# Performance work log

Hardware: AMD Instinct MI355X
Metric: run time of the kernel (lower is better)

## Reference

```python
import jax, jax.numpy as jnp
import numpy as np

B, S, D, H, F = 2, 2048, 1024, 16, 4096
DK = D // H
EPS = 1e-6


def _ln(x, g, b):
    mu = jnp.mean(x, axis=-1, keepdims=True)
    var = jnp.mean(jnp.square(x - mu), axis=-1, keepdims=True)
    return (x - mu) * jax.lax.rsqrt(var + EPS) * g + b


def setup_inputs() -> dict:
    key = jax.random.key(0)
    ks = jax.random.split(key, 8)
    sc = 0.02
    return {
        "x": jax.random.normal(ks[0], (B, S, D), jnp.float32),
        "wq": jax.random.normal(ks[1], (D, D), jnp.float32) * sc,
        "bq": jnp.zeros((D,), jnp.float32),
        "wk": jax.random.normal(ks[2], (D, D), jnp.float32) * sc,
        "bk": jnp.zeros((D,), jnp.float32),
        "wv": jax.random.normal(ks[3], (D, D), jnp.float32) * sc,
        "bv": jnp.zeros((D,), jnp.float32),
        "wo": jax.random.normal(ks[4], (D, D), jnp.float32) * sc,
        "bo": jnp.zeros((D,), jnp.float32),
        "w1": jax.random.normal(ks[5], (D, F), jnp.float32) * sc,
        "b1": jnp.zeros((F,), jnp.float32),
        "w2": jax.random.normal(ks[6], (F, D), jnp.float32) * sc,
        "b2": jnp.zeros((D,), jnp.float32),
        "g1": jnp.ones((D,), jnp.float32),
        "be1": jnp.zeros((D,), jnp.float32),
        "g2": jnp.ones((D,), jnp.float32),
        "be2": jnp.zeros((D,), jnp.float32),
    }


def reference(x, wq, bq, wk, bk, wv, bv, wo, bo, w1, b1, w2, b2, g1, be1, g2, be2):
    # Multi-head self-attention (no masks, eval-mode dropout = identity)
    q = (x @ wq + bq).reshape(B, S, H, DK)
    k = (x @ wk + bk).reshape(B, S, H, DK)
    v = (x @ wv + bv).reshape(B, S, H, DK)
    scale = 1.0 / (DK ** 0.5)
    score = jnp.einsum('bihd,bjhd->bhij', q, k) * scale  # [B,H,S,S]
    p = jax.nn.softmax(score, axis=-1)
    attn = jnp.einsum('bhij,bjhd->bihd', p, v).reshape(B, S, D)
    attn = attn @ wo + bo
    # residual + LayerNorm 1
    h = _ln(x + attn, g1, be1)
    # FFN (relu) + residual + LayerNorm 2
    ff = jax.nn.relu(h @ w1 + b1) @ w2 + b2
    return _ln(h + ff, g2, be2)
```

## Files before the change

kernel.cpp:

```cpp
#include <hip/hip_runtime.h>
#include <hip/hip_bf16.h>
#include <cmath>

typedef __bf16 bf16_t;
typedef __bf16 bf16x4 __attribute__((ext_vector_type(4)));
typedef __bf16 bf16x8 __attribute__((ext_vector_type(8)));
typedef float  f32x4  __attribute__((ext_vector_type(4)));

__device__ __forceinline__ void gld_lds16(const bf16_t* g, bf16_t* l) {
    __builtin_amdgcn_global_load_lds(
        (const __attribute__((address_space(1))) void*)g,
        (__attribute__((address_space(3))) void*)l,
        16, 0, 0);
}

struct PrepArgs {
    const float* w[6]; bf16_t* wt[6];
    int K[6], N[6], start[6];
    const float* x; bf16_t* xb; int castStart;
    const float* bq; const float* bk; float* bqkv; int biasStart;
};

__global__ __launch_bounds__(256) void prep(PrepArgs pa) {
    __shared__ float tile[32][33];
    const int bid = blockIdx.x, t = threadIdx.x;
    if (bid < pa.castStart) {
        int mi = 0;
#pragma unroll
        for (int i = 1; i < 6; i++) if (bid >= pa.start[i]) mi = i;
        const int tt  = bid - pa.start[mi];
        const int nbx = pa.N[mi] >> 5;
        const int n0 = (tt % nbx) * 32, k0 = (tt / nbx) * 32;
        const float* in = pa.w[mi];
        bf16_t* out = pa.wt[mi];
        const int K = pa.K[mi], N = pa.N[mi];
        const int tx = t & 31, ty = t >> 5;
#pragma unroll
        for (int i = 0; i < 4; i++) {
            int kk = ty + i * 8;
            tile[kk][tx] = in[(size_t)(k0 + kk) * N + n0 + tx];
        }
        __syncthreads();
#pragma unroll
        for (int i = 0; i < 4; i++) {
            int nn = ty + i * 8;
            out[(size_t)(n0 + nn) * K + k0 + tx] = (bf16_t)tile[tx][nn];
        }
    } else if (bid < pa.biasStart) {
        int i = (bid - pa.castStart) * 256 + t;
        f32x4 v = ((const f32x4*)pa.x)[i];
        bf16x4 o;
        o[0] = (bf16_t)v[0]; o[1] = (bf16_t)v[1]; o[2] = (bf16_t)v[2]; o[3] = (bf16_t)v[3];
        ((bf16x4*)pa.xb)[i] = o;
    } else {
#pragma unroll
        for (int j = 0; j < 8; j++) {
            int idx = t * 8 + j;
            pa.bqkv[idx] = idx < 1024 ? pa.bq[idx] : pa.bk[idx - 1024];
        }
    }
}

struct GemmDesc {
    const bf16_t* A; const bf16_t* Bt; const float* bias;
    float* Cf; bf16_t* Cb;
    int M, N, lda, Kloc, relu, nbn, bias_row;
    long bt_bstride, c_bstride;
    int scale_cols; float scale;
};

template<int MT>
__device__ __forceinline__ void gemm_core(const GemmDesc& d, int bidx, int batch,
                                          int kh, bf16_t* As, bf16_t* Bs) {
    constexpr int TM = MT * 32;
    const int tid  = threadIdx.x;
    const int lane = tid & 63;
    const int wave = tid >> 6;
    const int wm = wave & 1, wn = wave >> 1;

    const int span  = 8 * d.nbn;
    const int group = bidx / span;
    const int rem   = bidx % span;
    const int bm    = group * 8 + (rem & 7);
    const int bn    = rem >> 3;

    const bf16_t* Bt_b = d.Bt + (size_t)batch * d.bt_bstride;
    float*  Cf_b = d.Cf ? d.Cf + (size_t)batch * d.c_bstride + (size_t)kh * d.M * d.N : nullptr;
    bf16_t* Cb_b = d.Cb ? d.Cb + (size_t)batch * d.c_bstride : nullptr;
    const int koff = kh * d.Kloc;

    const int r4 = tid >> 2;
    const int kc = (tid & 3) * 8;
    const bf16_t* Ag = d.A  + (size_t)(bm * TM  + r4) * d.lda + koff + kc;
    const bf16_t* Bg = Bt_b + (size_t)(bn * 128 + r4) * d.lda + koff + kc;

    f32x4 acc[MT][4] = {};
    const int mrow = lane & 15;
    const int q8   = (lane >> 4) * 8;

    for (int k0 = 0; k0 < d.Kloc; k0 += 64) {
        __syncthreads();
#pragma unroll
        for (int hh = 0; hh < 2; hh++) {
#pragma unroll
            for (int i = 0; i < MT / 2; i++)
                gld_lds16(Ag + (size_t)(i * 64) * d.lda + k0 + hh * 32,
                          As + hh * (TM * 32) + i * 64 * 32 + tid * 8);
            gld_lds16(Bg + k0 + hh * 32,                      Bs + hh * 4096 + tid * 8);
            gld_lds16(Bg + (size_t)64 * d.lda + k0 + hh * 32, Bs + hh * 4096 + 64 * 32 + tid * 8);
        }
        __syncthreads();

#pragma unroll
        for (int hh = 0; hh < 2; hh++) {
            bf16x8 af[MT], bfr[4];
#pragma unroll
            for (int mt = 0; mt < MT; mt++)
                af[mt] = *(const bf16x8*)(As + hh * (TM * 32) +
                                          (wm * (MT * 16) + mt * 16 + mrow) * 32 + q8);
#pragma unroll
            for (int nt = 0; nt < 4; nt++)
                bfr[nt] = *(const bf16x8*)(Bs + hh * 4096 +
                                           (wn * 64 + nt * 16 + mrow) * 32 + q8);
#pragma unroll
            for (int mt = 0; mt < MT; mt++)
#pragma unroll
                for (int nt = 0; nt < 4; nt++)
                    acc[mt][nt] = __builtin_amdgcn_mfma_f32_16x16x32_bf16(
                        af[mt], bfr[nt], acc[mt][nt], 0, 0, 0);
        }
    }

    const int rq = (lane >> 4) * 4;
#pragma unroll
    for (int mt = 0; mt < MT; mt++) {
        int row0 = bm * TM + wm * (MT * 16) + mt * 16 + rq;
#pragma unroll
        for (int nt = 0; nt < 4; nt++) {
            int col = bn * 128 + wn * 64 + nt * 16 + mrow;
            float bvc = (d.bias && kh == 0 && !d.bias_row) ? d.bias[col] : 0.f;
            float sc = (col < d.scale_cols) ? d.scale : 1.f;
#pragma unroll
            for (int r = 0; r < 4; r++) {
                float bb = (d.bias && kh == 0 && d.bias_row) ? d.bias[row0 + r] : bvc;
                float v = acc[mt][nt][r] + bb;
                if (d.relu) v = fmaxf(v, 0.f);
                v *= sc;
                size_t idx = (size_t)(row0 + r) * d.N + col;
                if (Cf_b) Cf_b[idx] = v;
                if (Cb_b) Cb_b[idx] = (bf16_t)v;
            }
        }
    }
}

template<int MT>
__global__ __launch_bounds__(256) void gemm_bt(GemmDesc d) {
    __shared__ __attribute__((aligned(16))) bf16_t As[2 * MT * 32 * 32];
    __shared__ __attribute__((aligned(16))) bf16_t Bs[2 * 128 * 32];
    gemm_core<MT>(d, blockIdx.x, blockIdx.y, blockIdx.z, As, Bs);
}

__global__ __launch_bounds__(256) void gemm_dual(GemmDesc d0, int nblocks0,
                                                 GemmDesc d1, int nblocks1) {
    __shared__ __attribute__((aligned(16))) bf16_t As[2 * 128 * 32];
    __shared__ __attribute__((aligned(16))) bf16_t Bs[2 * 128 * 32];
    const int bid = blockIdx.x;
    if (bid < nblocks0) {
        gemm_core<4>(d0, bid, 0, 0, As, Bs);
    } else {
        int b2 = bid - nblocks0;
        gemm_core<4>(d1, b2 % nblocks1, b2 / nblocks1, 0, As, Bs);
    }
}

__global__ __launch_bounds__(512) void flash_attn_mfma(
    const bf16_t* __restrict__ QKb,
    const bf16_t* __restrict__ Vtg,
    bf16_t* __restrict__ Outb) {
    __shared__ __attribute__((aligned(16))) bf16_t QPs[128 * 72];
    __shared__ __attribute__((aligned(16))) bf16_t Ks[2][64 * 32];
    __shared__ __attribute__((aligned(16))) bf16_t Vs[2][64 * 32];
    const int t = threadIdx.x;
    const int lane = t & 63, wave = t >> 6;
    const int g = lane >> 4, cl = lane & 15;
    const int b = blockIdx.z, h = blockIdx.y, q0 = blockIdx.x * 128;
    const int RS = 2048;
    const bf16_t* Qg = QKb + (size_t)(b * 2048 + q0) * RS + h * 64;
    const bf16_t* Kg = QKb + (size_t)(b * 2048) * RS + 1024 + h * 64;
    const bf16_t* Vg = Vtg + ((size_t)b * 1024 + h * 64) * 2048;

    {
        int qr = t >> 2, qc = (t & 3) * 8;
        gld_lds16(Qg + (size_t)qr * RS + qc,      QPs + t * 8);
        gld_lds16(Qg + (size_t)qr * RS + 32 + qc, QPs + 4096 + t * 8);
    }
    const int kr = (t & 255) >> 2;
    const int kc = (t & 3) * 8;
    const int khf = (t >> 8) * 32;

    f32x4 Oacc[4] = {};
    f32x4 Lacc = {};
    bf16x8 ones;
#pragma unroll
    for (int j = 0; j < 8; j++) ones[j] = (bf16_t)1.0f;

    const int qrow_s = (wave * 16 + cl) * 32 + g * 8;
    const int prow_w = (wave * 16 + cl) * 72;

    __syncthreads();
    const bf16x8 bq0 = *(const bf16x8*)(QPs + qrow_s);
    const bf16x8 bq1 = *(const bf16x8*)(QPs + 4096 + qrow_s);

    for (int kt = 0; kt < 2048; kt += 64) {
        __syncthreads();
        gld_lds16(Kg + (size_t)(kt + kr) * RS + khf + kc,  (bf16_t*)Ks + t * 8);
        gld_lds16(Vg + (size_t)kr * 2048 + kt + khf + kc,  (bf16_t*)Vs + t * 8);
        __syncthreads();

        f32x4 Sacc[4] = {};
#pragma unroll
        for (int ks = 0; ks < 2; ks++) {
            const bf16x8 bq = ks ? bq1 : bq0;
#pragma unroll
            for (int mt = 0; mt < 4; mt++) {
                bf16x8 ak = *(const bf16x8*)(&Ks[ks][(mt * 16 + cl) * 32 + g * 8]);
                Sacc[mt] = __builtin_amdgcn_mfma_f32_16x16x32_bf16(ak, bq, Sacc[mt], 0, 0, 0);
            }
        }

#pragma unroll
        for (int mt = 0; mt < 4; mt++) {
            bf16x4 p4;
#pragma unroll
            for (int r = 0; r < 4; r++)
                p4[r] = (bf16_t)__builtin_amdgcn_exp2f(Sacc[mt][r]);
            *(bf16x4*)(QPs + prow_w + mt * 16 + g * 4) = p4;
        }

#pragma unroll
        for (int ks = 0; ks < 2; ks++) {
            bf16x8 ap = *(const bf16x8*)(QPs + prow_w + ks * 32 + g * 8);
            Lacc = __builtin_amdgcn_mfma_f32_16x16x32_bf16(ap, ones, Lacc, 0, 0, 0);
#pragma unroll
            for (int nt = 0; nt < 4; nt++) {
                bf16x8 bv = *(const bf16x8*)(&Vs[ks][(nt * 16 + cl) * 32 + g * 8]);
                Oacc[nt] = __builtin_amdgcn_mfma_f32_16x16x32_bf16(ap, bv, Oacc[nt], 0, 0, 0);
            }
        }
    }

#pragma unroll
    for (int r = 0; r < 4; r++) {
        float inv = 1.f / Lacc[r];
        int qrow = q0 + wave * 16 + g * 4 + r;
        size_t base = (size_t)(b * 2048 + qrow) * 1024 + h * 64;
#pragma unroll
        for (int nt = 0; nt < 4; nt++)
            Outb[base + nt * 16 + cl] = (bf16_t)(Oacc[nt][r] * inv);
    }
}

__global__ __launch_bounds__(256) void resid_ln3(const float* __restrict__ a,
                                                 const float* __restrict__ p0,
                                                 const float* __restrict__ p1,
                                                 const float* __restrict__ g,
                                                 const float* __restrict__ be,
                                                 float* __restrict__ outf,
                                                 bf16_t* __restrict__ outb) {
    const int row = blockIdx.x, t = threadIdx.x;
    const size_t base = (size_t)row * 1024;
    f32x4 v = ((const f32x4*)(a + base))[t] + ((const f32x4*)(p0 + base))[t];
    if (p1) v += ((const f32x4*)(p1 + base))[t];
    float sum = v[0] + v[1] + v[2] + v[3];
    float sq  = v[0] * v[0] + v[1] * v[1] + v[2] * v[2] + v[3] * v[3];
#pragma unroll
    for (int o = 1; o < 64; o <<= 1) {
        sum += __shfl_xor(sum, o);
        sq  += __shfl_xor(sq, o);
    }
    __shared__ float red[8];
    int wave = t >> 6, lane = t & 63;
    if (lane == 0) { red[wave] = sum; red[4 + wave] = sq; }
    __syncthreads();
    sum = red[0] + red[1] + red[2] + red[3];
    sq  = red[4] + red[5] + red[6] + red[7];
    float mu  = sum * (1.f / 1024.f);
    float var = sq * (1.f / 1024.f) - mu * mu;
    float rs  = rsqrtf(var + 1e-6f);
    f32x4 g4 = ((const f32x4*)g)[t];
    f32x4 b4 = ((const f32x4*)be)[t];
    f32x4 o = (v - mu) * rs * g4 + b4;
    ((f32x4*)(outf + base))[t] = o;
    if (outb) {
        bf16x4 ob;
        ob[0] = (bf16_t)o[0]; ob[1] = (bf16_t)o[1]; ob[2] = (bf16_t)o[2]; ob[3] = (bf16_t)o[3];
        ((bf16x4*)(outb + base))[t] = ob;
    }
}

extern "C" void kernel_launch(void* const* d_in, const int* in_sizes, int n_in,
                              void* d_out, int out_size, void* d_ws, size_t ws_size,
                              hipStream_t stream) {
    (void)in_sizes; (void)n_in; (void)out_size; (void)ws_size;
    const float* x   = (const float*)d_in[0];
    const float* wq  = (const float*)d_in[1];
    const float* bq  = (const float*)d_in[2];
    const float* wk  = (const float*)d_in[3];
    const float* bk  = (const float*)d_in[4];
    const float* wv  = (const float*)d_in[5];
    const float* bv  = (const float*)d_in[6];
    const float* wo  = (const float*)d_in[7];
    const float* bo  = (const float*)d_in[8];
    const float* w1  = (const float*)d_in[9];
    const float* b1  = (const float*)d_in[10];
    const float* w2  = (const float*)d_in[11];
    const float* b2  = (const float*)d_in[12];
    const float* g1  = (const float*)d_in[13];
    const float* be1 = (const float*)d_in[14];
    const float* g2  = (const float*)d_in[15];
    const float* be2 = (const float*)d_in[16];
    float* out = (float*)d_out;

    char* ws = (char*)d_ws;
    const size_t MB = 1ull << 20;
    bf16_t* xb    = (bf16_t*)(ws + 0);
    bf16_t* WtQKV = (bf16_t*)(ws + 8 * MB);
    bf16_t* WtO   = (bf16_t*)(ws + 14 * MB);
    bf16_t* Wt1   = (bf16_t*)(ws + 16 * MB);
    bf16_t* Wt2   = (bf16_t*)(ws + 24 * MB);
    float*  bqkv  = (float*)(ws + 32 * MB);
    bf16_t* QKb   = (bf16_t*)(ws + 33 * MB);
    bf16_t* Vt    = (bf16_t*)(ws + 49 * MB);
    bf16_t* ffb   = (bf16_t*)(ws + 33 * MB);
    float*  oa    = (float*)(ws + 65 * MB);
    float*  f2    = (float*)(ws + 65 * MB);
    float*  hbuf  = (float*)(ws + 97 * MB);
    bf16_t* hb    = (bf16_t*)(ws + 113 * MB);
    bf16_t* ab    = xb;
    const int MN = 4096 * 1024;
    const float Cs = 0.125f * 1.4426950408889634f;

    PrepArgs pa;
    pa.w[0] = wq; pa.w[1] = wk; pa.w[2] = wv; pa.w[3] = wo; pa.w[4] = w1; pa.w[5] = w2;
    pa.wt[0] = WtQKV; pa.wt[1] = WtQKV + 1024 * 1024; pa.wt[2] = WtQKV + 2048 * 1024;
    pa.wt[3] = WtO; pa.wt[4] = Wt1; pa.wt[5] = Wt2;
    int Ksz[6] = {1024, 1024, 1024, 1024, 1024, 4096};
    int Nsz[6] = {1024, 1024, 1024, 1024, 4096, 1024};
    int st[6]  = {0, 1024, 2048, 3072, 4096, 8192};
    for (int i = 0; i < 6; i++) { pa.K[i] = Ksz[i]; pa.N[i] = Nsz[i]; pa.start[i] = st[i]; }
    pa.x = x; pa.xb = xb; pa.castStart = 12288;
    pa.bq = bq; pa.bk = bk; pa.bqkv = bqkv; pa.biasStart = 12288 + 4096;
    prep<<<12288 + 4096 + 1, 256, 0, stream>>>(pa);

    GemmDesc dqk = { xb, WtQKV, bqkv, nullptr, QKb,
                     4096, 2048, 1024, 1024, 0, 16, 0, 0, 0, 1024, Cs };
    GemmDesc dv  = { WtQKV + 2048 * 1024, xb, bv, nullptr, Vt,
                     1024, 2048, 1024, 1024, 0, 16, 1,
                     (long)2048 * 1024, (long)1024 * 2048, 0, 1.f };
    gemm_dual<<<768, 256, 0, stream>>>(dqk, 512, dv, 128);

    flash_attn_mfma<<<dim3(16, 16, 2), 512, 0, stream>>>(QKb, Vt, ab);

    GemmDesc dwo = { ab, WtO, bo, oa, nullptr,
                     4096, 1024, 1024, 512, 0, 8, 0, 0, 0, 0, 1.f };
    gemm_bt<4><<<dim3(256, 1, 2), 256, 0, stream>>>(dwo);

    resid_ln3<<<4096, 256, 0, stream>>>(x, oa, oa + MN, g1, be1, hbuf, hb);

    GemmDesc df1 = { hb, Wt1, b1, nullptr, ffb,
                     4096, 4096, 1024, 1024, 1, 32, 0, 0, 0, 0, 1.f };
    gemm_bt<4><<<1024, 256, 0, stream>>>(df1);

    GemmDesc df2 = { ffb, Wt2, b2, f2, nullptr,
                     4096, 1024, 4096, 2048, 0, 8, 0, 0, 0, 0, 1.f };
    gemm_bt<4><<<dim3(256, 1, 2), 256, 0, stream>>>(df2);

    resid_ln3<<<4096, 256, 0, stream>>>(hbuf, f2, f2 + MN, g2, be2, out, nullptr);
}
```

Before: 418.7 us.

## Prefetch next GEMM K-tile into registers while computing current tile

Replaces the direct global-to-LDS loads with register prefetching: the next K-tile is loaded into registers before the MFMA loop and written to LDS after a barrier. The goal is to hide global memory latency behind matrix compute in a single-buffered LDS scheme. In exchange it uses more VGPRs and adds explicit LDS store instructions, and it drops the async global_load_lds path, which may reduce occupancy.

```diff
diff --git a/kernel.cpp b/kernel.cpp
--- a/kernel.cpp
+++ b/kernel.cpp
@@ -98,18 +98,39 @@
     const int mrow = lane & 15;
     const int q8   = (lane >> 4) * 8;
 
+    bf16x8 pA[MT / 2][2], pB[2][2];
+
+#define LOAD_TILE(K0)                                                          \
+    {                                                                          \
+        _Pragma("unroll")                                                      \
+        for (int hh = 0; hh < 2; hh++) {                                       \
+            _Pragma("unroll")                                                  \
+            for (int i = 0; i < MT / 2; i++)                                   \
+                pA[i][hh] = *(const bf16x8*)(Ag + (size_t)(i * 64) * d.lda +   \
+                                             (K0) + hh * 32);                  \
+            pB[0][hh] = *(const bf16x8*)(Bg + (K0) + hh * 32);                 \
+            pB[1][hh] = *(const bf16x8*)(Bg + (size_t)64 * d.lda + (K0) + hh * 32); \
+        }                                                                      \
+    }
+#define STORE_TILE()                                                           \
+    {                                                                          \
+        _Pragma("unroll")                                                      \
+        for (int hh = 0; hh < 2; hh++) {                                       \
+            _Pragma("unroll")                                                  \
+            for (int i = 0; i < MT / 2; i++)                                   \
+                *(bf16x8*)(As + hh * (TM * 32) + i * 64 * 32 + tid * 8) = pA[i][hh]; \
+            *(bf16x8*)(Bs + hh * 4096 + tid * 8) = pB[0][hh];                  \
+            *(bf16x8*)(Bs + hh * 4096 + 64 * 32 + tid * 8) = pB[1][hh];        \
+        }                                                                      \
+    }
+
+    LOAD_TILE(0);
+    STORE_TILE();
+
     for (int k0 = 0; k0 < d.Kloc; k0 += 64) {
         __syncthreads();
-#pragma unroll
-        for (int hh = 0; hh < 2; hh++) {
-#pragma unroll
-            for (int i = 0; i < MT / 2; i++)
-                gld_lds16(Ag + (size_t)(i * 64) * d.lda + k0 + hh * 32,
-                          As + hh * (TM * 32) + i * 64 * 32 + tid * 8);
-            gld_lds16(Bg + k0 + hh * 32,                      Bs + hh * 4096 + tid * 8);
-            gld_lds16(Bg + (size_t)64 * d.lda + k0 + hh * 32, Bs + hh * 4096 + 64 * 32 + tid * 8);
-        }
-        __syncthreads();
+        const bool more = (k0 + 64 < d.Kloc);
+        if (more) LOAD_TILE(k0 + 64);
 
 #pragma unroll
         for (int hh = 0; hh < 2; hh++) {
@@ -129,7 +150,12 @@
                     acc[mt][nt] = __builtin_amdgcn_mfma_f32_16x16x32_bf16(
                         af[mt], bfr[nt], acc[mt][nt], 0, 0, 0);
         }
-    }
+
+        __syncthreads();
+        if (more) STORE_TILE();
+    }
+#undef LOAD_TILE
+#undef STORE_TILE
 
     const int rq = (lane >> 4) * 4;
 #pragma unroll
```

Result: no change. 414.3 us (-1.0%).
